# Performance work log

Hardware: AMD Instinct MI355X
Metric: run time of the kernel (lower is better)

The kernel has to match this reference:

```python
import jax, jax.numpy as jnp
import numpy as np

B, S, D = 2, 2048, 2048
H, KV, HD = 32, 8, 64          # n_heads, n_kv_heads, head_dim
REP = H // KV                  # 4
THETA = 10000.0


def _rotate_half(u):
    h = u.shape[-1] // 2
    return jnp.concatenate([-u[..., h:], u[..., :h]], axis=-1)


def setup_inputs() -> dict:
    key = jax.random.key(0)
    ks = jax.random.split(key, 5)
    x = jax.random.normal(ks[0], (B, S, D), dtype=jnp.float32)
    Wq = jax.random.normal(ks[1], (D, H * HD), dtype=jnp.float32) * 0.02
    Wk = jax.random.normal(ks[2], (D, KV * HD), dtype=jnp.float32) * 0.02
    Wv = jax.random.normal(ks[3], (D, KV * HD), dtype=jnp.float32) * 0.02
    Wo = jax.random.normal(ks[4], (H * HD, D), dtype=jnp.float32) * 0.02
    return {"x": x, "Wq": Wq, "Wk": Wk, "Wv": Wv, "Wo": Wo}


def reference(x, Wq, Wk, Wv, Wo):
    b, s, d = x.shape
    # QKV projections (nn.Linear, no bias)
    q = (x @ Wq).reshape(b, s, H, HD).transpose(0, 2, 1, 3)   # [B,H,S,HD]
    k = (x @ Wk).reshape(b, s, KV, HD).transpose(0, 2, 1, 3)  # [B,KV,S,HD]
    v = (x @ Wv).reshape(b, s, KV, HD).transpose(0, 2, 1, 3)  # [B,KV,S,HD]

    # RoPE (position_offset = 0)
    inv_freq = 1.0 / (THETA ** (jnp.arange(0, HD, 2, dtype=jnp.float32) / HD))
    freqs = jnp.outer(jnp.arange(s, dtype=jnp.float32), inv_freq)  # [S,HD/2]
    emb = jnp.concatenate([freqs, freqs], axis=-1)                  # [S,HD]
    cos, sin = jnp.cos(emb), jnp.sin(emb)
    q = q * cos + _rotate_half(q) * sin
    k = k * cos + _rotate_half(k) * sin

    # Grouped attention: avoid materializing repeated KV tensors.
    qg = q.reshape(b, KV, REP, s, HD)                               # [B,KV,REP,S,HD]
    scale = 1.0 / np.sqrt(HD)
    scores = jnp.einsum('bgrqd,bgkd->bgrqk', qg, k) * scale         # [B,KV,REP,S,S]
    causal = jnp.tril(jnp.ones((s, s), dtype=bool))
    scores = jnp.where(causal, scores, jnp.finfo(jnp.float32).min)
    probs = jax.nn.softmax(scores.astype(jnp.float32), axis=-1).astype(q.dtype)
    out = jnp.einsum('bgrqk,bgkd->bgrqd', probs, v)                 # [B,KV,REP,S,HD]
    out = out.reshape(b, H, s, HD).transpose(0, 2, 1, 3).reshape(b, s, H * HD)
    return out @ Wo                                                  # [B,S,D]
```

## Files before the change

kernel.cpp:

```cpp
#include <hip/hip_runtime.h>
#include <math.h>

typedef __bf16 bf16_t;
typedef bf16_t bf16x8 __attribute__((ext_vector_type(8)));
typedef bf16_t bf16x4 __attribute__((ext_vector_type(4)));
typedef float floatx4 __attribute__((ext_vector_type(4)));

#define MFMA16(a, b, c) __builtin_amdgcn_mfma_f32_16x16x32_bf16((a), (b), (c), 0, 0, 0)

__device__ __forceinline__ void gld16(const void* g, void* lds)
{
    __builtin_amdgcn_global_load_lds(
        reinterpret_cast<const __attribute__((address_space(1))) void*>(
            reinterpret_cast<uintptr_t>(g)),
        reinterpret_cast<__attribute__((address_space(3))) void*>(
            (unsigned int)reinterpret_cast<uintptr_t>(lds)),
        16, 0, 0);
}

template <typename TC>
__device__ __forceinline__ void gemm_bt_body(
    const bf16_t* __restrict__ A, const bf16_t* __restrict__ Bt,
    TC* __restrict__ C, int row0, int col0, int N, int K,
    bf16_t* As, bf16_t* Bs)
{
    const int tid  = threadIdx.x;
    const int wave = tid >> 6, lane = tid & 63;
    const int quad = lane >> 4, l16 = lane & 15;
    const int wm = (wave >> 1) * 64, wn = (wave & 1) * 64;

    floatx4 acc[4][4] = {};

    for (int k0 = 0; k0 < K; k0 += 64) {
        __syncthreads();
        #pragma unroll
        for (int i = 0; i < 4; ++i) {
            int c = i * 256 + tid;
            int r = c >> 3, s = c & 7;
            int ks = k0 + ((s ^ (r & 7)) << 3);
            gld16(A  + (size_t)(row0 + r) * K + ks, &As[(i * 256 + wave * 64) * 8]);
            gld16(Bt + (size_t)(col0 + r) * K + ks, &Bs[(i * 256 + wave * 64) * 8]);
        }
        __syncthreads();
        #pragma unroll
        for (int kh = 0; kh < 2; ++kh) {
            bf16x8 af[4], bfr[4];
            #pragma unroll
            for (int t = 0; t < 4; ++t) {
                int ar = wm + t * 16 + l16;
                af[t]  = *(const bf16x8*)&As[ar * 64 + (((kh * 4 + quad) ^ (ar & 7)) << 3)];
                int br = wn + t * 16 + l16;
                bfr[t] = *(const bf16x8*)&Bs[br * 64 + (((kh * 4 + quad) ^ (br & 7)) << 3)];
            }
            #pragma unroll
            for (int mt = 0; mt < 4; ++mt)
                #pragma unroll
                for (int nt = 0; nt < 4; ++nt)
                    acc[mt][nt] = MFMA16(af[mt], bfr[nt], acc[mt][nt]);
        }
    }
    #pragma unroll
    for (int mt = 0; mt < 4; ++mt)
        #pragma unroll
        for (int nt = 0; nt < 4; ++nt)
            #pragma unroll
            for (int r = 0; r < 4; ++r)
                C[(size_t)(row0 + wm + mt * 16 + quad * 4 + r) * N
                  + col0 + wn + nt * 16 + l16] = (TC)acc[mt][nt][r];
}

template <typename TC>
__global__ __launch_bounds__(256) void gemm_bt(
    const bf16_t* __restrict__ A, const bf16_t* __restrict__ Bt,
    TC* __restrict__ C, int N, int K)
{
    __shared__ bf16_t As[128 * 64];
    __shared__ bf16_t Bs[128 * 64];
    gemm_bt_body<TC>(A, Bt, C, blockIdx.y * 128, blockIdx.x * 128, N, K, As, Bs);
}

__global__ __launch_bounds__(256) void gemm_qkv(
    const bf16_t* __restrict__ A, const bf16_t* __restrict__ BtQ,
    const bf16_t* __restrict__ BtK, const bf16_t* __restrict__ BtV,
    bf16_t* __restrict__ CQ, bf16_t* __restrict__ CK, bf16_t* __restrict__ CV)
{
    __shared__ bf16_t As[128 * 64];
    __shared__ bf16_t Bs[128 * 64];
    const int x = blockIdx.x;
    const bf16_t* Bt; bf16_t* C; int N, col0;
    if (x < 16)      { Bt = BtQ; C = CQ; N = 2048; col0 = x * 128; }
    else if (x < 20) { Bt = BtK; C = CK; N = 512;  col0 = (x - 16) * 128; }
    else             { Bt = BtV; C = CV; N = 512;  col0 = (x - 20) * 128; }
    gemm_bt_body<bf16_t>(A, Bt, C, blockIdx.y * 128, col0, N, 2048, As, Bs);
}

__global__ __launch_bounds__(256) void conv_bf16_k(
    const float* __restrict__ in, bf16_t* __restrict__ o, int n4)
{
    int i = blockIdx.x * 256 + threadIdx.x;
    if (i >= n4) return;
    float4 f = ((const float4*)in)[i];
    bf16x4 v = {(bf16_t)f.x, (bf16_t)f.y, (bf16_t)f.z, (bf16_t)f.w};
    ((bf16x4*)o)[i] = v;
}

__global__ __launch_bounds__(256) void transpose_conv_k(
    const float* __restrict__ W, bf16_t* __restrict__ Wt, int K, int N)
{
    __shared__ float t[32][33];
    int bx = blockIdx.x * 32, by = blockIdx.y * 32;
    int tx = threadIdx.x & 31, ty = threadIdx.x >> 5;
    #pragma unroll
    for (int i = 0; i < 32; i += 8)
        t[ty + i][tx] = W[(size_t)(by + ty + i) * N + bx + tx];
    __syncthreads();
    #pragma unroll
    for (int i = 0; i < 32; i += 8)
        Wt[(size_t)(bx + ty + i) * K + by + tx] = (bf16_t)t[tx][ty + i];
}

__global__ __launch_bounds__(256) void transpose_v_k(
    const bf16_t* __restrict__ V, bf16_t* __restrict__ Vt)
{
    __shared__ bf16_t t[32][34];
    int b  = blockIdx.z;
    int bx = blockIdx.x * 32, by = blockIdx.y * 32;
    int tx = threadIdx.x & 31, ty = threadIdx.x >> 5;
    #pragma unroll
    for (int i = 0; i < 32; i += 8)
        t[ty + i][tx] = V[((size_t)b * 2048 + by + ty + i) * 512 + bx + tx];
    __syncthreads();
    #pragma unroll
    for (int i = 0; i < 32; i += 8)
        Vt[((size_t)b * 512 + bx + ty + i) * 2048 + by + tx] = t[tx][ty + i];
}

__global__ __launch_bounds__(256) void rope_bf16(bf16_t* __restrict__ p, int nheads, int total)
{
    int idx = blockIdx.x * 256 + threadIdx.x;
    if (idx >= total) return;
    int i   = idx & 31;
    int h   = (idx >> 5) % nheads;
    int row = idx / (32 * nheads);
    int pos = row & 2047;
    float invf = powf(10000.0f, -(float)i / 32.0f);
    float sv, cv;
    sincosf((float)pos * invf, &sv, &cv);
    size_t base = (size_t)row * ((size_t)nheads * 64) + (size_t)h * 64 + i;
    float a  = (float)p[base];
    float b2 = (float)p[base + 32];
    p[base]      = (bf16_t)(a * cv - b2 * sv);
    p[base + 32] = (bf16_t)(b2 * cv + a * sv);
}

__global__ __launch_bounds__(256) void gqa_attn(
    const bf16_t* __restrict__ Q, const bf16_t* __restrict__ Kc,
    const bf16_t* __restrict__ Vt, bf16_t* __restrict__ AO)
{
    __shared__ bf16_t Ks[2][64 * 64];
    __shared__ bf16_t Vs[2][64 * 64];
    __shared__ bf16_t Ps[4][32 * 64];

    const int x = blockIdx.x, h = blockIdx.y, b = blockIdx.z, g = h >> 2;
    const int tid  = threadIdx.x;
    const int wave = tid >> 6, lane = tid & 63;
    const int quad = lane >> 4, l16 = lane & 15;

    #pragma unroll 1
    for (int t = 0; t < 2; ++t) {
        const int qt = t ? x : (15 - x);
        const int q0 = qt * 128;
        int qb[2];
        qb[0] = q0 + wave * 16;
        qb[1] = qb[0] + 64;

        bf16x8 qf[2][2];
        #pragma unroll
        for (int mt = 0; mt < 2; ++mt) {
            int qrow = qb[mt] + l16;
            const bf16_t* qp = Q + (size_t)(b * 2048 + qrow) * 2048 + h * 64 + quad * 8;
            bf16x8 lo = *(const bf16x8*)qp;
            bf16x8 hi = *(const bf16x8*)(qp + 32);
            #pragma unroll
            for (int j = 0; j < 8; ++j) {
                int d = quad * 8 + j;
                float invf = powf(10000.0f, -(float)d / 32.0f);
                float sv, cv;
                sincosf((float)qrow * invf, &sv, &cv);
                float a = (float)lo[j], c2 = (float)hi[j];
                qf[mt][0][j] = (bf16_t)((a * cv - c2 * sv) * 0.125f);
                qf[mt][1][j] = (bf16_t)((c2 * cv + a * sv) * 0.125f);
            }
        }

        floatx4 o[2][4] = {};
        float lsum[2][4] = {};

        const int ktmax = 2 * qt + 1;

        __asm__ volatile("s_waitcnt lgkmcnt(0)" ::: "memory");
        __builtin_amdgcn_s_barrier();
        #pragma unroll
        for (int i = 0; i < 2; ++i) {
            int c = i * 256 + tid;
            int r = c >> 3, s = c & 7;
            int sw = (s ^ (r & 7)) << 3;
            gld16(Kc + (size_t)(b * 2048 + r) * 512 + g * 64 + sw,
                  &Ks[0][(i * 256 + wave * 64) * 8]);
            gld16(Vt + (size_t)(b * 512 + g * 64 + r) * 2048 + sw,
                  &Vs[0][(i * 256 + wave * 64) * 8]);
        }

        #pragma unroll 1
        for (int kt = 0; kt <= ktmax; ++kt) {
            const int cur = kt & 1;
            if (kt < ktmax) {
                const int kn = kt + 1;
                #pragma unroll
                for (int i = 0; i < 2; ++i) {
                    int c = i * 256 + tid;
                    int r = c >> 3, s = c & 7;
                    int sw = (s ^ (r & 7)) << 3;
                    gld16(Kc + (size_t)(b * 2048 + kn * 64 + r) * 512 + g * 64 + sw,
                          &Ks[cur ^ 1][(i * 256 + wave * 64) * 8]);
                    gld16(Vt + (size_t)(b * 512 + g * 64 + r) * 2048 + kn * 64 + sw,
                          &Vs[cur ^ 1][(i * 256 + wave * 64) * 8]);
                }
                __asm__ volatile("s_waitcnt vmcnt(4)" ::: "memory");
            } else {
                __asm__ volatile("s_waitcnt vmcnt(0)" ::: "memory");
            }
            __builtin_amdgcn_s_barrier();

            bool en[2];
            en[0] = (kt * 64) <= (qb[0] + 15);
            en[1] = (kt * 64) <= (qb[1] + 15);

            floatx4 sc[2][4] = {};
            #pragma unroll
            for (int nt = 0; nt < 4; ++nt)
                #pragma unroll
                for (int kh = 0; kh < 2; ++kh) {
                    int kr = nt * 16 + l16;
                    bf16x8 kf = *(const bf16x8*)&Ks[cur][kr * 64
                                  + (((kh * 4 + quad) ^ (kr & 7)) << 3)];
                    if (en[0]) sc[0][nt] = MFMA16(qf[0][kh], kf, sc[0][nt]);
                    if (en[1]) sc[1][nt] = MFMA16(qf[1][kh], kf, sc[1][nt]);
                }

            #pragma unroll
            for (int mt = 0; mt < 2; ++mt) {
                if (!en[mt]) continue;
                if (kt * 64 + 63 > qb[mt]) {
                    #pragma unroll
                    for (int nt = 0; nt < 4; ++nt)
                        #pragma unroll
                        for (int r = 0; r < 4; ++r) {
                            int ka = kt * 64 + nt * 16 + l16;
                            int qa = qb[mt] + quad * 4 + r;
                            if (ka > qa) sc[mt][nt][r] = -1e30f;
                        }
                }
                #pragma unroll
                for (int nt = 0; nt < 4; ++nt)
                    #pragma unroll
                    for (int r = 0; r < 4; ++r) {
                        float pv = __expf(fminf(sc[mt][nt][r], 60.0f));
                        lsum[mt][r] += pv;
                        int lq = mt * 16 + quad * 4 + r;
                        int s  = (nt * 2 + (l16 >> 3)) ^ (lq & 7);
                        Ps[wave][lq * 64 + s * 8 + (l16 & 7)] = (bf16_t)pv;
                    }
            }
            __builtin_amdgcn_wave_barrier();
            __asm__ volatile("s_waitcnt lgkmcnt(0)" ::: "memory");
            __builtin_amdgcn_wave_barrier();

            #pragma unroll
            for (int kh = 0; kh < 2; ++kh) {
                bf16x8 pf[2];
                #pragma unroll
                for (int mt = 0; mt < 2; ++mt)
                    if (en[mt])
                        pf[mt] = *(const bf16x8*)&Ps[wave][(mt * 16 + l16) * 64
                                   + (((kh * 4 + quad) ^ (l16 & 7)) << 3)];
                #pragma unroll
                for (int nt = 0; nt < 4; ++nt) {
                    int vr = nt * 16 + l16;
                    bf16x8 vf = *(const bf16x8*)&Vs[cur][vr * 64
                                  + (((kh * 4 + quad) ^ (vr & 7)) << 3)];
                    if (en[0]) o[0][nt] = MFMA16(pf[0], vf, o[0][nt]);
                    if (en[1]) o[1][nt] = MFMA16(pf[1], vf, o[1][nt]);
                }
            }
            __asm__ volatile("s_waitcnt lgkmcnt(0)" ::: "memory");
            __builtin_amdgcn_s_barrier();
        }

        #pragma unroll
        for (int mt = 0; mt < 2; ++mt) {
            float ls[4];
            #pragma unroll
            for (int r = 0; r < 4; ++r) ls[r] = lsum[mt][r];
            #pragma unroll
            for (int off = 1; off < 16; off <<= 1)
                #pragma unroll
                for (int r = 0; r < 4; ++r)
                    ls[r] += __shfl_xor(ls[r], off, 64);
            float rcp[4];
            #pragma unroll
            for (int r = 0; r < 4; ++r) rcp[r] = 1.0f / ls[r];
            #pragma unroll
            for (int nt = 0; nt < 4; ++nt)
                #pragma unroll
                for (int r = 0; r < 4; ++r)
                    AO[(size_t)(b * 2048 + qb[mt] + quad * 4 + r) * 2048
                       + h * 64 + nt * 16 + l16] = (bf16_t)(o[mt][nt][r] * rcp[r]);
        }
    }
}

extern "C" void kernel_launch(void* const* d_in, const int* in_sizes, int n_in,
                              void* d_out, int out_size, void* d_ws, size_t ws_size,
                              hipStream_t stream)
{
    const float* x  = (const float*)d_in[0];
    const float* Wq = (const float*)d_in[1];
    const float* Wk = (const float*)d_in[2];
    const float* Wv = (const float*)d_in[3];
    const float* Wo = (const float*)d_in[4];
    float* out = (float*)d_out;

    const size_t MB = 1024 * 1024;
    char* ws = (char*)d_ws;
    bf16_t* xb_AO = (bf16_t*)(ws);
    bf16_t* WqoT  = (bf16_t*)(ws + 16 * MB);
    bf16_t* WkT   = (bf16_t*)(ws + 24 * MB);
    bf16_t* WvT   = (bf16_t*)(ws + 26 * MB);
    bf16_t* Qw    = (bf16_t*)(ws + 28 * MB);
    bf16_t* Kw    = (bf16_t*)(ws + 44 * MB);
    bf16_t* Vw    = (bf16_t*)(ws + 48 * MB);
    bf16_t* VtG   = (bf16_t*)(ws + 52 * MB);

    conv_bf16_k<<<8192, 256, 0, stream>>>(x, xb_AO, 2097152);
    transpose_conv_k<<<dim3(64, 64), 256, 0, stream>>>(Wq, WqoT, 2048, 2048);
    transpose_conv_k<<<dim3(16, 64), 256, 0, stream>>>(Wk, WkT, 2048, 512);
    transpose_conv_k<<<dim3(16, 64), 256, 0, stream>>>(Wv, WvT, 2048, 512);

    gemm_qkv<<<dim3(24, 32), 256, 0, stream>>>(xb_AO, WqoT, WkT, WvT, Qw, Kw, Vw);

    rope_bf16<<<4096, 256, 0, stream>>>(Kw, 8, 4096 * 8 * 32);
    transpose_v_k<<<dim3(16, 64, 2), 256, 0, stream>>>(Vw, VtG);
    transpose_conv_k<<<dim3(64, 64), 256, 0, stream>>>(Wo, WqoT, 2048, 2048);

    gqa_attn<<<dim3(8, 32, 2), 256, 0, stream>>>(Qw, Kw, VtG, xb_AO);

    gemm_bt<float><<<dim3(16, 32), 256, 0, stream>>>(xb_AO, WqoT, out, 2048, 2048);
}
```

Baseline: 341.7 us.

## Keep attention probabilities in registers via transposed MFMA and merge prep kernels

The attention kernel now computes S^T with K as the A operand, so the exponentiated probabilities land in a register layout that feeds the PV MFMA directly. This drops the per-wave LDS round trip for P. It also uses exp2 with the log2e factor folded into the Q scale and vectorises the output stores. Separately, the small conversion, transpose and RoPE kernels are merged into two launches to cut launch overhead. The cost is reliance on the k16 MFMA builtin or lane shuffles, and the removal of the score clamp.

```diff
diff --git a/kernel.cpp b/kernel.cpp
--- a/kernel.cpp
+++ b/kernel.cpp
@@ -5,8 +5,30 @@
 typedef bf16_t bf16x8 __attribute__((ext_vector_type(8)));
 typedef bf16_t bf16x4 __attribute__((ext_vector_type(4)));
 typedef float floatx4 __attribute__((ext_vector_type(4)));
+typedef short short4v __attribute__((ext_vector_type(4)));
 
 #define MFMA16(a, b, c) __builtin_amdgcn_mfma_f32_16x16x32_bf16((a), (b), (c), 0, 0, 0)
+
+#if __has_builtin(__builtin_amdgcn_exp2f)
+#define PEXP(x) __builtin_amdgcn_exp2f(x)
+#define SCORE_SCALE (0.125f * 1.4426950408889634f)
+#else
+#define PEXP(x) __expf(x)
+#define SCORE_SCALE 0.125f
+#endif
+
+#if __has_builtin(__builtin_amdgcn_mfma_f32_16x16x16bf16_1k)
+#define HAVE_MFMA_K16 1
+__device__ __forceinline__ floatx4 mfma_k16(bf16x4 a, bf16x4 b, floatx4 c)
+{
+    union { bf16x4 v; short4v s; } ua, ub;
+    ua.v = a; ub.v = b;
+    return __builtin_amdgcn_mfma_f32_16x16x16bf16_1k(ua.s, ub.s, c, 0, 0, 0);
+}
+#endif
+
+union PU { unsigned u[2]; bf16x4 v; };
+union BU { unsigned u[4]; bf16x8 v; };
 
 __device__ __forceinline__ void gld16(const void* g, void* lds)
 {
@@ -94,22 +116,11 @@
     gemm_bt_body<bf16_t>(A, Bt, C, blockIdx.y * 128, col0, N, 2048, As, Bs);
 }
 
-__global__ __launch_bounds__(256) void conv_bf16_k(
-    const float* __restrict__ in, bf16_t* __restrict__ o, int n4)
-{
-    int i = blockIdx.x * 256 + threadIdx.x;
-    if (i >= n4) return;
-    float4 f = ((const float4*)in)[i];
-    bf16x4 v = {(bf16_t)f.x, (bf16_t)f.y, (bf16_t)f.z, (bf16_t)f.w};
-    ((bf16x4*)o)[i] = v;
-}
-
-__global__ __launch_bounds__(256) void transpose_conv_k(
-    const float* __restrict__ W, bf16_t* __restrict__ Wt, int K, int N)
-{
-    __shared__ float t[32][33];
-    int bx = blockIdx.x * 32, by = blockIdx.y * 32;
-    int tx = threadIdx.x & 31, ty = threadIdx.x >> 5;
+__device__ __forceinline__ void transpose_body(
+    const float* __restrict__ W, bf16_t* __restrict__ Wt, int K, int N,
+    int bx, int by, float (*t)[33], int tid)
+{
+    int tx = tid & 31, ty = tid >> 5;
     #pragma unroll
     for (int i = 0; i < 32; i += 8)
         t[ty + i][tx] = W[(size_t)(by + ty + i) * N + bx + tx];
@@ -119,47 +130,77 @@
         Wt[(size_t)(bx + ty + i) * K + by + tx] = (bf16_t)t[tx][ty + i];
 }
 
-__global__ __launch_bounds__(256) void transpose_v_k(
-    const bf16_t* __restrict__ V, bf16_t* __restrict__ Vt)
-{
-    __shared__ bf16_t t[32][34];
-    int b  = blockIdx.z;
-    int bx = blockIdx.x * 32, by = blockIdx.y * 32;
-    int tx = threadIdx.x & 31, ty = threadIdx.x >> 5;
-    #pragma unroll
-    for (int i = 0; i < 32; i += 8)
-        t[ty + i][tx] = V[((size_t)b * 2048 + by + ty + i) * 512 + bx + tx];
-    __syncthreads();
-    #pragma unroll
-    for (int i = 0; i < 32; i += 8)
-        Vt[((size_t)b * 512 + bx + ty + i) * 2048 + by + tx] = t[tx][ty + i];
-}
-
-__global__ __launch_bounds__(256) void rope_bf16(bf16_t* __restrict__ p, int nheads, int total)
-{
-    int idx = blockIdx.x * 256 + threadIdx.x;
-    if (idx >= total) return;
-    int i   = idx & 31;
-    int h   = (idx >> 5) % nheads;
-    int row = idx / (32 * nheads);
-    int pos = row & 2047;
-    float invf = powf(10000.0f, -(float)i / 32.0f);
-    float sv, cv;
-    sincosf((float)pos * invf, &sv, &cv);
-    size_t base = (size_t)row * ((size_t)nheads * 64) + (size_t)h * 64 + i;
-    float a  = (float)p[base];
-    float b2 = (float)p[base + 32];
-    p[base]      = (bf16_t)(a * cv - b2 * sv);
-    p[base + 32] = (bf16_t)(b2 * cv + a * sv);
+__global__ __launch_bounds__(256) void prep_all(
+    const float* __restrict__ x, const float* __restrict__ Wq,
+    const float* __restrict__ Wk, const float* __restrict__ Wv,
+    bf16_t* __restrict__ xb, bf16_t* __restrict__ WqT,
+    bf16_t* __restrict__ WkT, bf16_t* __restrict__ WvT)
+{
+    __shared__ float t[32][33];
+    const int blk = blockIdx.x, tid = threadIdx.x;
+    if (blk < 8192) {
+        int i = blk * 256 + tid;
+        float4 f = ((const float4*)x)[i];
+        bf16x4 v = {(bf16_t)f.x, (bf16_t)f.y, (bf16_t)f.z, (bf16_t)f.w};
+        ((bf16x4*)xb)[i] = v;
+    } else if (blk < 12288) {
+        int r = blk - 8192;
+        transpose_body(Wq, WqT, 2048, 2048, (r & 63) * 32, (r >> 6) * 32, t, tid);
+    } else if (blk < 13312) {
+        int r = blk - 12288;
+        transpose_body(Wk, WkT, 2048, 512, (r & 15) * 32, (r >> 4) * 32, t, tid);
+    } else {
+        int r = blk - 13312;
+        transpose_body(Wv, WvT, 2048, 512, (r & 15) * 32, (r >> 4) * 32, t, tid);
+    }
+}
+
+__global__ __launch_bounds__(256) void mid_all(
+    bf16_t* __restrict__ Kw, const bf16_t* __restrict__ Vw,
+    bf16_t* __restrict__ VtG, const float* __restrict__ Wo,
+    bf16_t* __restrict__ WoT)
+{
+    __shared__ float tf[32][33];
+    __shared__ bf16_t tb[32][34];
+    const int blk = blockIdx.x, tid = threadIdx.x;
+    if (blk < 4096) {
+        int idx = blk * 256 + tid;
+        int i   = idx & 31;
+        int h   = (idx >> 5) & 7;
+        int row = idx >> 8;
+        int pos = row & 2047;
+        float invf = powf(10000.0f, -(float)i / 32.0f);
+        float sv, cv;
+        sincosf((float)pos * invf, &sv, &cv);
+        size_t base = (size_t)row * 512 + (size_t)h * 64 + i;
+        float a  = (float)Kw[base];
+        float b2 = (float)Kw[base + 32];
+        Kw[base]      = (bf16_t)(a * cv - b2 * sv);
+        Kw[base + 32] = (bf16_t)(b2 * cv + a * sv);
+    } else if (blk < 6144) {
+        int r  = blk - 4096;
+        int bz = r >> 10, r2 = r & 1023;
+        int bx = (r2 & 15) * 32, by = (r2 >> 4) * 32;
+        int tx = tid & 31, ty = tid >> 5;
+        #pragma unroll
+        for (int i = 0; i < 32; i += 8)
+            tb[ty + i][tx] = Vw[((size_t)bz * 2048 + by + ty + i) * 512 + bx + tx];
+        __syncthreads();
+        #pragma unroll
+        for (int i = 0; i < 32; i += 8)
+            VtG[((size_t)bz * 512 + bx + ty + i) * 2048 + by + tx] = tb[tx][ty + i];
+    } else {
+        int r = blk - 6144;
+        transpose_body(Wo, WoT, 2048, 2048, (r & 63) * 32, (r >> 6) * 32, tf, tid);
+    }
 }
 
 __global__ __launch_bounds__(256) void gqa_attn(
     const bf16_t* __restrict__ Q, const bf16_t* __restrict__ Kc,
     const bf16_t* __restrict__ Vt, bf16_t* __restrict__ AO)
 {
-    __shared__ bf16_t Ks[2][64 * 64];
-    __shared__ bf16_t Vs[2][64 * 64];
-    __shared__ bf16_t Ps[4][32 * 64];
+    __shared__ alignas(16) bf16_t Ks[2][64 * 64];
+    __shared__ alignas(16) bf16_t Vs[2][64 * 64];
 
     const int x = blockIdx.x, h = blockIdx.y, b = blockIdx.z, g = h >> 2;
     const int tid  = threadIdx.x;
@@ -188,13 +229,13 @@
                 float sv, cv;
                 sincosf((float)qrow * invf, &sv, &cv);
                 float a = (float)lo[j], c2 = (float)hi[j];
-                qf[mt][0][j] = (bf16_t)((a * cv - c2 * sv) * 0.125f);
-                qf[mt][1][j] = (bf16_t)((c2 * cv + a * sv) * 0.125f);
+                qf[mt][0][j] = (bf16_t)((a * cv - c2 * sv) * SCORE_SCALE);
+                qf[mt][1][j] = (bf16_t)((c2 * cv + a * sv) * SCORE_SCALE);
             }
         }
 
         floatx4 o[2][4] = {};
-        float lsum[2][4] = {};
+        floatx4 ls4[2] = {};
 
         const int ktmax = 2 * qt + 1;
 
@@ -236,86 +277,100 @@
             en[0] = (kt * 64) <= (qb[0] + 15);
             en[1] = (kt * 64) <= (qb[1] + 15);
 
-            floatx4 sc[2][4] = {};
-            #pragma unroll
-            for (int nt = 0; nt < 4; ++nt)
-                #pragma unroll
-                for (int kh = 0; kh < 2; ++kh) {
-                    int kr = nt * 16 + l16;
-                    bf16x8 kf = *(const bf16x8*)&Ks[cur][kr * 64
-                                  + (((kh * 4 + quad) ^ (kr & 7)) << 3)];
-                    if (en[0]) sc[0][nt] = MFMA16(qf[0][kh], kf, sc[0][nt]);
-                    if (en[1]) sc[1][nt] = MFMA16(qf[1][kh], kf, sc[1][nt]);
-                }
-
+            floatx4 st[2][4] = {};
+            #pragma unroll
+            for (int nt = 0; nt < 4; ++nt) {
+                int kr = nt * 16 + l16;
+                bf16x8 kf0 = *(const bf16x8*)&Ks[cur][kr * 64 + ((quad ^ (kr & 7)) << 3)];
+                bf16x8 kf1 = *(const bf16x8*)&Ks[cur][kr * 64 + (((4 + quad) ^ (kr & 7)) << 3)];
+                if (en[0]) {
+                    st[0][nt] = MFMA16(kf0, qf[0][0], st[0][nt]);
+                    st[0][nt] = MFMA16(kf1, qf[0][1], st[0][nt]);
+                }
+                if (en[1]) {
+                    st[1][nt] = MFMA16(kf0, qf[1][0], st[1][nt]);
+                    st[1][nt] = MFMA16(kf1, qf[1][1], st[1][nt]);
+                }
+            }
+
+            PU pk[2][4];
             #pragma unroll
             for (int mt = 0; mt < 2; ++mt) {
                 if (!en[mt]) continue;
-                if (kt * 64 + 63 > qb[mt]) {
-                    #pragma unroll
-                    for (int nt = 0; nt < 4; ++nt)
-                        #pragma unroll
-                        for (int r = 0; r < 4; ++r) {
-                            int ka = kt * 64 + nt * 16 + l16;
-                            int qa = qb[mt] + quad * 4 + r;
-                            if (ka > qa) sc[mt][nt][r] = -1e30f;
-                        }
-                }
-                #pragma unroll
-                for (int nt = 0; nt < 4; ++nt)
+                const bool diag = (kt * 64 + 63) > qb[mt];
+                const int qa = qb[mt] + l16;
+                #pragma unroll
+                for (int nt = 0; nt < 4; ++nt) {
+                    float pv[4];
                     #pragma unroll
                     for (int r = 0; r < 4; ++r) {
-                        float pv = __expf(fminf(sc[mt][nt][r], 60.0f));
-                        lsum[mt][r] += pv;
-                        int lq = mt * 16 + quad * 4 + r;
-                        int s  = (nt * 2 + (l16 >> 3)) ^ (lq & 7);
-                        Ps[wave][lq * 64 + s * 8 + (l16 & 7)] = (bf16_t)pv;
+                        float e = PEXP(st[mt][nt][r]);
+                        if (diag) {
+                            int ka = kt * 64 + nt * 16 + quad * 4 + r;
+                            if (ka > qa) e = 0.f;
+                        }
+                        ls4[mt][r] += e;
+                        pv[r] = e;
                     }
-            }
-            __builtin_amdgcn_wave_barrier();
-            __asm__ volatile("s_waitcnt lgkmcnt(0)" ::: "memory");
-            __builtin_amdgcn_wave_barrier();
-
-            #pragma unroll
-            for (int kh = 0; kh < 2; ++kh) {
-                bf16x8 pf[2];
-                #pragma unroll
-                for (int mt = 0; mt < 2; ++mt)
-                    if (en[mt])
-                        pf[mt] = *(const bf16x8*)&Ps[wave][(mt * 16 + l16) * 64
-                                   + (((kh * 4 + quad) ^ (l16 & 7)) << 3)];
-                #pragma unroll
-                for (int nt = 0; nt < 4; ++nt) {
-                    int vr = nt * 16 + l16;
-                    bf16x8 vf = *(const bf16x8*)&Vs[cur][vr * 64
-                                  + (((kh * 4 + quad) ^ (vr & 7)) << 3)];
-                    if (en[0]) o[0][nt] = MFMA16(pf[0], vf, o[0][nt]);
-                    if (en[1]) o[1][nt] = MFMA16(pf[1], vf, o[1][nt]);
-                }
-            }
+                    pk[mt][nt].v = bf16x4{(bf16_t)pv[0], (bf16_t)pv[1],
+                                          (bf16_t)pv[2], (bf16_t)pv[3]};
+                }
+            }
+
+#ifdef HAVE_MFMA_K16
+            #pragma unroll
+            for (int nt = 0; nt < 4; ++nt)
+                #pragma unroll
+                for (int dt = 0; dt < 4; ++dt) {
+                    int vr = dt * 16 + l16;
+                    int slot = ((nt << 1) | (quad >> 1)) ^ (vr & 7);
+                    bf16x4 va = *(const bf16x4*)&Vs[cur][vr * 64 + (slot << 3)
+                                                         + ((quad & 1) << 2)];
+                    if (en[0]) o[0][dt] = mfma_k16(va, pk[0][nt].v, o[0][dt]);
+                    if (en[1]) o[1][dt] = mfma_k16(va, pk[1][nt].v, o[1][dt]);
+                }
+#else
+            #pragma unroll
+            for (int H = 0; H < 2; ++H) {
+                BU bfv[2];
+                #pragma unroll
+                for (int mt = 0; mt < 2; ++mt) {
+                    if (!en[mt]) continue;
+                    #pragma unroll
+                    for (int j = 0; j < 4; ++j) {
+                        int srcl = (((quad & 1) << 1) + (j >> 1)) * 16 + l16;
+                        unsigned a0 = (unsigned)__shfl((int)pk[mt][2 * H].u[j & 1], srcl, 64);
+                        unsigned a1 = (unsigned)__shfl((int)pk[mt][2 * H + 1].u[j & 1], srcl, 64);
+                        bfv[mt].u[j] = (quad >> 1) ? a1 : a0;
+                    }
+                }
+                #pragma unroll
+                for (int dt = 0; dt < 4; ++dt) {
+                    int vr = dt * 16 + l16;
+                    bf16x8 va = *(const bf16x8*)&Vs[cur][vr * 64
+                                  + ((((H << 2) | quad) ^ (vr & 7)) << 3)];
+                    if (en[0]) o[0][dt] = MFMA16(va, bfv[0].v, o[0][dt]);
+                    if (en[1]) o[1][dt] = MFMA16(va, bfv[1].v, o[1][dt]);
+                }
+            }
+#endif
             __asm__ volatile("s_waitcnt lgkmcnt(0)" ::: "memory");
             __builtin_amdgcn_s_barrier();
         }
 
         #pragma unroll
         for (int mt = 0; mt < 2; ++mt) {
-            float ls[4];
-            #pragma unroll
-            for (int r = 0; r < 4; ++r) ls[r] = lsum[mt][r];
-            #pragma unroll
-            for (int off = 1; off < 16; off <<= 1)
-                #pragma unroll
-                for (int r = 0; r < 4; ++r)
-                    ls[r] += __shfl_xor(ls[r], off, 64);
-            float rcp[4];
-            #pragma unroll
-            for (int r = 0; r < 4; ++r) rcp[r] = 1.0f / ls[r];
-            #pragma unroll
-            for (int nt = 0; nt < 4; ++nt)
-                #pragma unroll
-                for (int r = 0; r < 4; ++r)
-                    AO[(size_t)(b * 2048 + qb[mt] + quad * 4 + r) * 2048
-                       + h * 64 + nt * 16 + l16] = (bf16_t)(o[mt][nt][r] * rcp[r]);
+            float l = ls4[mt][0] + ls4[mt][1] + ls4[mt][2] + ls4[mt][3];
+            l += __shfl_xor(l, 16, 64);
+            l += __shfl_xor(l, 32, 64);
+            float rc = 1.0f / l;
+            #pragma unroll
+            for (int dt = 0; dt < 4; ++dt) {
+                bf16x4 ov = {(bf16_t)(o[mt][dt][0] * rc), (bf16_t)(o[mt][dt][1] * rc),
+                             (bf16_t)(o[mt][dt][2] * rc), (bf16_t)(o[mt][dt][3] * rc)};
+                *(bf16x4*)&AO[(size_t)(b * 2048 + qb[mt] + l16) * 2048
+                              + h * 64 + dt * 16 + quad * 4] = ov;
+            }
         }
     }
 }
@@ -342,16 +397,11 @@
     bf16_t* Vw    = (bf16_t*)(ws + 48 * MB);
     bf16_t* VtG   = (bf16_t*)(ws + 52 * MB);
 
-    conv_bf16_k<<<8192, 256, 0, stream>>>(x, xb_AO, 2097152);
-    transpose_conv_k<<<dim3(64, 64), 256, 0, stream>>>(Wq, WqoT, 2048, 2048);
-    transpose_conv_k<<<dim3(16, 64), 256, 0, stream>>>(Wk, WkT, 2048, 512);
-    transpose_conv_k<<<dim3(16, 64), 256, 0, stream>>>(Wv, WvT, 2048, 512);
+    prep_all<<<14336, 256, 0, stream>>>(x, Wq, Wk, Wv, xb_AO, WqoT, WkT, WvT);
 
     gemm_qkv<<<dim3(24, 32), 256, 0, stream>>>(xb_AO, WqoT, WkT, WvT, Qw, Kw, Vw);
 
-    rope_bf16<<<4096, 256, 0, stream>>>(Kw, 8, 4096 * 8 * 32);
-    transpose_v_k<<<dim3(16, 64, 2), 256, 0, stream>>>(Vw, VtG);
-    transpose_conv_k<<<dim3(64, 64), 256, 0, stream>>>(Wo, WqoT, 2048, 2048);
+    mid_all<<<10240, 256, 0, stream>>>(Kw, Vw, VtG, Wo, WqoT);
 
     gqa_attn<<<dim3(8, 32, 2), 256, 0, stream>>>(Qw, Kw, VtG, xb_AO);
 
```

Result: faster. 327.5 us (-4.2%).
